# Kernel tuning notes

Measured on AMD Instinct MI355X. Metric: run time of the kernel, lower is better.

The kernel has to match this reference:

```python
import jax, jax.numpy as jnp
import numpy as np

N = 4096       # nodes
NFEAT = 256    # feature dim
NCLASS = 16
E = 65536      # edges = N * avg_degree(16)
NLAYER = 4
ALPHA = 0.5    # blancealpha (non-trainable)
LAMBDA_1 = 1.0
LAMBDA_2 = 1.0
EPS = 1e-12    # F.normalize eps


def setup_inputs() -> dict:
    key = jax.random.key(0)
    ks = jax.random.split(key, 9)
    feat = jax.random.normal(ks[0], (N, NFEAT), dtype=jnp.float32)
    z0 = jax.random.uniform(ks[1], (N, NFEAT), dtype=jnp.float32)       # torch.rand init of z
    w1 = jax.random.uniform(ks[2], (N, N), dtype=jnp.float32)           # uniform_(0,1)
    EA = jax.random.uniform(ks[3], (N, N), dtype=jnp.float32)           # uniform_(0,1)
    w2_w = jax.random.normal(ks[4], (2 * NFEAT, NCLASS), dtype=jnp.float32) * 0.05
    w2_b = jnp.zeros((NCLASS,), dtype=jnp.float32)
    edge_i = jax.random.randint(ks[5], (E,), 0, N, dtype=jnp.int32)
    edge_j = jax.random.randint(ks[6], (E,), 0, N, dtype=jnp.int32)
    edge_val = jax.random.uniform(ks[7], (E,), dtype=jnp.float32)
    # dense adjacency from the sparse edge list (coalesce -> duplicate indices sum)
    adj = jnp.zeros((N, N), dtype=jnp.float32).at[edge_i, edge_j].add(edge_val)
    # w22 = ones with zeros at edge positions (as in __init__)
    w22 = jnp.ones((N, N), dtype=jnp.float32).at[edge_i, edge_j].set(0.0)
    return dict(feat=feat, z0=z0, w1=w1, EA=EA, w2_w=w2_w, w2_b=w2_b,
                adj=adj, w22=w22, edge_val=edge_val, edge_i=edge_i, edge_j=edge_j)


def reference(feat, z0, w1, EA, w2_w, w2_b, adj, w22, edge_val, edge_i, edge_j):
    n = feat.shape[0]
    y = feat                      # y starts as feat
    z = z0                        # torch.rand init, passed in for determinism
    EP = jnp.ones((n, n), dtype=feat.dtype)
    masked_EA = ALPHA * EA * w22  # constant across layers
    for _ in range(NLAYER):
        # dropout is identity in eval mode (training=False)
        A = adj * EP + masked_EA            # [n, n]
        yyT = y @ y.T                       # [n, n] (reused; same values as the two torch.mm calls)
        temp = EP.T @ y + A @ y - yyT @ y   # [n, nfeat]
        temp = jax.nn.sigmoid(w1 @ temp)
        y_n = (LAMBDA_2 / 2) * temp + feat
        z_n = z - A @ z                     # (I - A) @ z
        # ans(z, adj): edgewise ||z_i - z_j|| * adj_val scattered to dense
        P = jnp.linalg.norm(z[edge_i] - z[edge_j], axis=1) * edge_val   # [E]
        M = jnp.zeros((n, n), dtype=z.dtype).at[edge_i, edge_j].add(P)
        EP = (LAMBDA_2 * (yyT - masked_EA) - LAMBDA_1 * 0.5 * M) / LAMBDA_2
        y, z = y_n, z_n
    # F.normalize(p=2, dim=1)
    y = y / jnp.maximum(jnp.linalg.norm(y, axis=1, keepdims=True), EPS)
    z = z / jnp.maximum(jnp.linalg.norm(z, axis=1, keepdims=True), EPS)
    p = jnp.concatenate([z, y], axis=1)     # [n, 2*nfeat]
    logits = p @ w2_w + w2_b
    return jax.nn.log_softmax(logits, axis=1)
```

## Files before the change

kernel.cpp:

```cpp
#include <hip/hip_runtime.h>

#define Nn 4096
#define Ff 256
#define NCLS 16
#define Ne 65536
#define TSZ 262144
#define NF (Nn*Ff)
#define NNx (Nn*Nn)

typedef unsigned short u16;
typedef unsigned int u32;
typedef __attribute__((ext_vector_type(8))) short short8;
typedef __attribute__((ext_vector_type(4))) float float4v;

__device__ __forceinline__ float bfh(u16 u){ return __uint_as_float(((u32)u)<<16); }
__device__ __forceinline__ u16 f2bf(float f){
    u32 u = __float_as_uint(f);
    return (u16)((u + 0x7FFFu + ((u>>16)&1u)) >> 16);
}
__device__ __forceinline__ void gload16(const u16* g, u16* l){
    __builtin_amdgcn_global_load_lds(
        (const __attribute__((address_space(1))) u32*)(const void*)g,
        (__attribute__((address_space(3))) u32*)(void*)l, 16, 0, 0);
}

__device__ float g_yA[NF], g_yB[NF], g_zA[NF], g_zB[NF], g_t1[NF], g_T1[NF];
__device__ float g_Gp[32*Ff*Ff], g_col[Ff], g_P[Ne], g_cc[Ne], g_hV[TSZ];
__device__ float g_pb[(size_t)24*NF];
__device__ u32 g_hK[TSZ], g_slot[Ne];
__device__ int g_cntI[Nn], g_cntJ[Nn], g_rpI[Nn+1], g_rpJ[Nn+1], g_fI[Nn], g_fJ[Nn];
__device__ int g_lI[Ne], g_lJ[Ne];
__device__ __align__(16) u16 g_w1h[NNx], g_w1l[NNx];
__device__ __align__(16) u16 g_meh[NNx], g_mel[NNx];
__device__ __align__(16) u16 g_mth[NNx], g_mtl[NNx];
__device__ __align__(16) u16 g_x0h[NF], g_x0l[NF], g_x1h[NF], g_x1l[NF];
__device__ __align__(16) u16 g_zt0h[NF], g_zt0l[NF], g_zt1h[NF], g_zt1l[NF];
__device__ __align__(16) u16 g_yr0h[NF], g_yr0l[NF], g_yr1h[NF], g_yr1l[NF];
__device__ __align__(16) u16 g_tth[NF], g_ttl[NF];
__device__ __align__(16) u16 g_gth[Ff*Ff], g_gtl[Ff*Ff];
__device__ __align__(16) u16 g_g2h[Ff*Ff], g_g2l[Ff*Ff];

__global__ __launch_bounds__(256) void k_zero(float* p, int n){
    int i = blockIdx.x*256 + threadIdx.x;
    if (i < n) p[i] = 0.f;
}
__global__ __launch_bounds__(256) void k_zeroi(int* p, int n){
    int i = blockIdx.x*256 + threadIdx.x;
    if (i < n) p[i] = 0;
}
__global__ __launch_bounds__(256) void k_fillc(float* p, float v, int n){
    int i = blockIdx.x*256 + threadIdx.x;
    if (i < n) p[i] = v;
}
__global__ __launch_bounds__(256) void k_hkeys_clear(u32* K){
    int i = blockIdx.x*256 + threadIdx.x;
    if (i < TSZ) K[i] = 0xFFFFFFFFu;
}
__global__ __launch_bounds__(256) void k_hsetup(u32* K, u32* slot, const int* ei, const int* ej){
    int e = blockIdx.x*256 + threadIdx.x;
    if (e >= Ne) return;
    u32 key = ((u32)ei[e] << 12) | (u32)ej[e];
    u32 h = (key * 2654435761u) & (TSZ-1);
    for (;;){
        u32 old = atomicCAS(&K[h], 0xFFFFFFFFu, key);
        if (old == 0xFFFFFFFFu || old == key){ slot[e] = h; break; }
        h = (h+1) & (TSZ-1);
    }
}

__global__ __launch_bounds__(256) void k_count(int* cntI, int* cntJ, const int* ei, const int* ej){
    int e = blockIdx.x*256 + threadIdx.x;
    if (e < Ne){ atomicAdd(&cntI[ei[e]], 1); atomicAdd(&cntJ[ej[e]], 1); }
}
__global__ __launch_bounds__(1024) void k_scan(const int* cnt, int* rp){
    __shared__ int s[1024];
    int t = threadIdx.x, b = t*4;
    int a0 = cnt[b], a1 = cnt[b+1], a2 = cnt[b+2], a3 = cnt[b+3];
    int sum = a0+a1+a2+a3;
    s[t] = sum; __syncthreads();
    for (int o = 1; o < 1024; o <<= 1){
        int v = (t >= o) ? s[t-o] : 0;
        __syncthreads();
        s[t] += v;
        __syncthreads();
    }
    int excl = s[t] - sum;
    rp[b] = excl; rp[b+1] = excl+a0; rp[b+2] = excl+a0+a1; rp[b+3] = excl+a0+a1+a2;
    if (t == 1023) rp[4096] = s[1023];
}
__global__ __launch_bounds__(256) void k_fillcsr(const int* rpI, const int* rpJ, int* fI, int* fJ,
                                                 int* lI, int* lJ, const int* ei, const int* ej){
    int e = blockIdx.x*256 + threadIdx.x;
    if (e >= Ne) return;
    int i = ei[e], j = ej[e];
    lI[rpI[i] + atomicAdd(&fI[i], 1)] = e;
    lJ[rpJ[j] + atomicAdd(&fJ[j], 1)] = e;
}

__global__ __launch_bounds__(256) void k_split4(ushort4* hi, ushort4* lo, const float4* w, int n4){
    int i = blockIdx.x*256 + threadIdx.x;
    if (i >= n4) return;
    float4 v = w[i];
    ushort4 h, l;
    h.x = f2bf(v.x); l.x = f2bf(v.x - bfh(h.x));
    h.y = f2bf(v.y); l.y = f2bf(v.y - bfh(h.y));
    h.z = f2bf(v.z); l.z = f2bf(v.z - bfh(h.z));
    h.w = f2bf(v.w); l.w = f2bf(v.w - bfh(h.w));
    hi[i] = h; lo[i] = l;
}
__global__ __launch_bounds__(256) void k_splitME2(u16* meh, u16* mel, u16* mth, u16* mtl,
                                                  const float* ea, const float* w22){
    __shared__ float T[64][65];
    int r0 = blockIdx.y*64, c0 = blockIdx.x*64;
    int c = threadIdx.x & 63, rr = threadIdx.x >> 6;
    for (int q = 0; q < 16; ++q){
        int r = q*4 + rr;
        size_t idx = (size_t)(r0+r)*Nn + c0 + c;
        float v = 0.5f*ea[idx]*w22[idx];
        T[r][c] = v;
        u16 h = f2bf(v); meh[idx] = h; mel[idx] = f2bf(v - bfh(h));
    }
    __syncthreads();
    for (int q = 0; q < 16; ++q){
        int r = q*4 + rr;
        float v = T[c][r];
        size_t o = (size_t)(c0+r)*Nn + r0 + c;
        u16 h = f2bf(v); mth[o] = h; mtl[o] = f2bf(v - bfh(h));
    }
}
__global__ __launch_bounds__(256) void k_splitXT(u16* hi, u16* lo, const float* X){
    __shared__ float T[64][65];
    int r0 = blockIdx.y*64, c0 = blockIdx.x*64;
    int c = threadIdx.x & 63, rr = threadIdx.x >> 6;
    for (int q = 0; q < 16; ++q){
        int r = q*4 + rr;
        T[r][c] = X[(size_t)(r0+r)*Ff + c0 + c];
    }
    __syncthreads();
    for (int q = 0; q < 16; ++q){
        int r = q*4 + rr;
        float v = T[c][r];
        size_t o = (size_t)(c0+r)*Nn + r0 + c;
        u16 h = f2bf(v); hi[o] = h; lo[o] = f2bf(v - bfh(h));
    }
}
__global__ __launch_bounds__(256) void k_splitGT(u16* hi, u16* lo, const float* Gp){
    __shared__ float T[64][65];
    int r0 = blockIdx.y*64, c0 = blockIdx.x*64;
    int c = threadIdx.x & 63, rr = threadIdx.x >> 6;
    for (int q = 0; q < 16; ++q){
        int r = q*4 + rr;
        float v = 0.f;
        #pragma unroll
        for (int z = 0; z < 16; ++z) v += Gp[z*(Ff*Ff) + (r0+r)*Ff + c0 + c];
        T[r][c] = v;
    }
    __syncthreads();
    for (int q = 0; q < 16; ++q){
        int r = q*4 + rr;
        float v = T[c][r];
        int o = (c0+r)*Ff + r0 + c;
        u16 h = f2bf(v); hi[o] = h; lo[o] = f2bf(v - bfh(h));
    }
}
__global__ __launch_bounds__(256) void k_splitGT2(u16* h0, u16* l0, u16* h1, u16* l1,
                                                  const float* Gp){
    __shared__ float T[64][65];
    const int which = blockIdx.z;
    u16* hi = which ? h1 : h0;
    u16* lo = which ? l1 : l0;
    const float* G = Gp + (size_t)which*16*(Ff*Ff);
    int r0 = blockIdx.y*64, c0 = blockIdx.x*64;
    int c = threadIdx.x & 63, rr = threadIdx.x >> 6;
    for (int q = 0; q < 16; ++q){
        int r = q*4 + rr;
        float v = 0.f;
        #pragma unroll
        for (int z = 0; z < 16; ++z) v += G[z*(Ff*Ff) + (r0+r)*Ff + c0 + c];
        T[r][c] = v;
    }
    __syncthreads();
    for (int q = 0; q < 16; ++q){
        int r = q*4 + rr;
        float v = T[c][r];
        int o = (c0+r)*Ff + r0 + c;
        u16 h = f2bf(v); hi[o] = h; lo[o] = f2bf(v - bfh(h));
    }
}

__device__ __forceinline__ void mm_tile(
    const u16* __restrict__ Ahp, const u16* __restrict__ Alp,
    const u16* __restrict__ Bhp, const u16* __restrict__ Blp,
    size_t sA, size_t sB, int i0, int j0, int k0,
    u16* LAh, u16* LAl, u16* LBh, u16* LBl,
    float4v* acc, int lane, int w)
{
    const int g1 = w*64 + lane;
    const int g2 = g1 + 256;
    const int r1 = g1>>3, p1 = g1&7, r2 = g2>>3, p2 = g2&7;
    const size_t a1 = (size_t)(i0+r1)*sA + (size_t)(k0 + ((p1 ^ (r1&7))<<3));
    const size_t a2 = (size_t)(i0+r2)*sA + (size_t)(k0 + ((p2 ^ (r2&7))<<3));
    const size_t b1 = (size_t)(j0+r1)*sB + (size_t)(k0 + ((p1 ^ (r1&7))<<3));
    const size_t b2 = (size_t)(j0+r2)*sB + (size_t)(k0 + ((p2 ^ (r2&7))<<3));
    __syncthreads();
    gload16(Ahp + a1, LAh + g1*8);
    gload16(Ahp + a2, LAh + g2*8);
    gload16(Alp + a1, LAl + g1*8);
    gload16(Alp + a2, LAl + g2*8);
    gload16(Bhp + b1, LBh + g1*8);
    gload16(Bhp + b2, LBh + g2*8);
    gload16(Blp + b1, LBl + g1*8);
    gload16(Blp + b2, LBl + g2*8);
    __syncthreads();
    const int arow = w*16 + (lane&15);
    const int aswz = arow & 7;
    #pragma unroll
    for (int kk = 0; kk < 2; ++kk){
        const int ch = kk*4 + (lane>>4);
        short8 ah = *(const short8*)(LAh + arow*64 + ((ch ^ aswz)<<3));
        short8 al = *(const short8*)(LAl + arow*64 + ((ch ^ aswz)<<3));
        #pragma unroll
        for (int c = 0; c < 4; ++c){
            const int brow = c*16 + (lane&15);
            const int bo = brow*64 + ((ch ^ (brow&7))<<3);
            short8 bh = *(const short8*)(LBh + bo);
            short8 bl = *(const short8*)(LBl + bo);
            acc[c] = __builtin_amdgcn_mfma_f32_16x16x32_bf16(ah, bh, acc[c], 0,0,0);
            acc[c] = __builtin_amdgcn_mfma_f32_16x16x32_bf16(ah, bl, acc[c], 0,0,0);
            acc[c] = __builtin_amdgcn_mfma_f32_16x16x32_bf16(al, bh, acc[c], 0,0,0);
        }
    }
}

template<int V>
__global__ __launch_bounds__(256) void k_mm(float* __restrict__ out,
        const u16* __restrict__ Ahp, const u16* __restrict__ Alp,
        const u16* __restrict__ Bhp, const u16* __restrict__ Blp,
        const float* __restrict__ aux1){
    __shared__ u16 LAh[4096], LAl[4096], LBh[4096], LBl[4096];
    const int tid = threadIdx.x, lane = tid & 63, w = tid >> 6;
    const int j0 = blockIdx.x*64, i0 = blockIdx.y*64;
    float4v acc[4];
    #pragma unroll
    for (int c = 0; c < 4; ++c) acc[c] = (float4v){0.f,0.f,0.f,0.f};
    for (int kt = 0; kt < 4; ++kt)
        mm_tile(Ahp, Alp, Bhp, Blp, (size_t)Ff, (size_t)Ff, i0, j0, kt*64, LAh, LAl, LBh, LBl, acc, lane, w);
    #pragma unroll
    for (int c = 0; c < 4; ++c)
        #pragma unroll
        for (int r = 0; r < 4; ++r){
            int grow = i0 + w*16 + (lane>>4)*4 + r;
            int gcol = j0 + c*16 + (lane&15);
            size_t idx = (size_t)grow*Ff + gcol;
            float v = acc[c][r];
            if constexpr (V == 3) out[idx] = aux1[idx] - v;
            if constexpr (V == 4) out[idx] = aux1[gcol] - v;
            if constexpr (V == 5) out[idx] = v;
        }
}

__global__ __launch_bounds__(256) void k_gram_mm(float* __restrict__ Gp,
        const u16* __restrict__ Ahp, const u16* __restrict__ Alp,
        const u16* __restrict__ Bhp, const u16* __restrict__ Blp){
    __shared__ u16 LAh[4096], LAl[4096], LBh[4096], LBl[4096];
    const int tid = threadIdx.x, lane = tid & 63, w = tid >> 6;
    const int j0 = blockIdx.x*64, i0 = blockIdx.y*64, kb = blockIdx.z*256;
    float4v acc[4];
    #pragma unroll
    for (int c = 0; c < 4; ++c) acc[c] = (float4v){0.f,0.f,0.f,0.f};
    for (int kt = 0; kt < 4; ++kt)
        mm_tile(Ahp, Alp, Bhp, Blp, (size_t)Nn, (size_t)Nn, i0, j0, kb + kt*64, LAh, LAl, LBh, LBl, acc, lane, w);
    float* op = Gp + (size_t)blockIdx.z*(Ff*Ff);
    #pragma unroll
    for (int c = 0; c < 4; ++c)
        #pragma unroll
        for (int r = 0; r < 4; ++r){
            int grow = i0 + w*16 + (lane>>4)*4 + r;
            int gcol = j0 + c*16 + (lane&15);
            op[grow*Ff + gcol] = acc[c][r];
        }
}

__global__ __launch_bounds__(256) void k_gram_mm2(float* __restrict__ Gp,
        const u16* __restrict__ Ahp, const u16* __restrict__ Alp,
        const u16* __restrict__ Bhp, const u16* __restrict__ Blp){
    __shared__ u16 LAh[4096], LAl[4096], LBh[4096], LBl[4096];
    const int tid = threadIdx.x, lane = tid & 63, w = tid >> 6;
    const int j0 = blockIdx.x*64, i0 = blockIdx.y*64;
    const int pz = blockIdx.z;
    const int kb = (pz & 15)*256, which = pz >> 4;
    const u16* pAh = which ? Bhp : Ahp;
    const u16* pAl = which ? Blp : Alp;
    float4v acc[4];
    #pragma unroll
    for (int c = 0; c < 4; ++c) acc[c] = (float4v){0.f,0.f,0.f,0.f};
    for (int kt = 0; kt < 4; ++kt)
        mm_tile(pAh, pAl, Bhp, Blp, (size_t)Nn, (size_t)Nn, i0, j0, kb + kt*64, LAh, LAl, LBh, LBl, acc, lane, w);
    float* op = Gp + (size_t)pz*(Ff*Ff);
    #pragma unroll
    for (int c = 0; c < 4; ++c)
        #pragma unroll
        for (int r = 0; r < 4; ++r){
            int grow = i0 + w*16 + (lane>>4)*4 + r;
            int gcol = j0 + c*16 + (lane&15);
            op[grow*Ff + gcol] = acc[c][r];
        }
}

template<int KSP>
__global__ __launch_bounds__(512) void k_mmB(float* __restrict__ pb,
        const u16* __restrict__ A0h, const u16* __restrict__ A0l,
        const u16* __restrict__ B0h, const u16* __restrict__ B0l,
        const u16* __restrict__ A1h, const u16* __restrict__ A1l,
        const u16* __restrict__ B1h, const u16* __restrict__ B1l,
        const u16* __restrict__ A2h, const u16* __restrict__ A2l,
        const u16* __restrict__ B2h, const u16* __restrict__ B2l){
    __shared__ u16 LAh[4096], LAl[4096], LBh[16384], LBl[16384];
    const int tid = threadIdx.x, lane = tid & 63, w = tid >> 6;
    const int z = blockIdx.x, i0 = blockIdx.y*64, bat = blockIdx.z;
    const u16 *Ah, *Al, *Bh, *Bl;
    if (bat == 0){ Ah = A0h; Al = A0l; Bh = B0h; Bl = B0l; }
    else if (bat == 1){ Ah = A1h; Al = A1l; Bh = B1h; Bl = B1l; }
    else { Ah = A2h; Al = A2l; Bh = B2h; Bl = B2l; }
    const int wr = w >> 2, wc = w & 3;
    float4v acc[2][4];
    #pragma unroll
    for (int m = 0; m < 2; ++m)
        #pragma unroll
        for (int n = 0; n < 4; ++n) acc[m][n] = (float4v){0.f,0.f,0.f,0.f};

    const int ra = tid >> 3, pa = tid & 7;
    const size_t aoff = (size_t)(i0+ra)*Nn + (size_t)((pa ^ (ra&7))<<3);
    constexpr int NKT = 64 / KSP;

    for (int kt = 0; kt < NKT; ++kt){
        const int k0 = z*(NKT*64) + kt*64;
        __syncthreads();
        gload16(Ah + aoff + k0, LAh + tid*8);
        gload16(Al + aoff + k0, LAl + tid*8);
        #pragma unroll
        for (int it = 0; it < 4; ++it){
            int g = it*512 + tid;
            int r = g >> 3, p = g & 7;
            size_t b = (size_t)r*Nn + (size_t)(k0 + ((p ^ (r&7))<<3));
            gload16(Bh + b, LBh + g*8);
            gload16(Bl + b, LBl + g*8);
        }
        __syncthreads();
        #pragma unroll
        for (int kk = 0; kk < 2; ++kk){
            const int ch = kk*4 + (lane>>4);
            short8 ah0, ah1, al0, al1;
            {
                const int arow = wr*32 + (lane&15);
                const int ao = arow*64 + ((ch ^ (arow&7))<<3);
                ah0 = *(const short8*)(LAh + ao);
                al0 = *(const short8*)(LAl + ao);
            }
            {
                const int arow = wr*32 + 16 + (lane&15);
                const int ao = arow*64 + ((ch ^ (arow&7))<<3);
                ah1 = *(const short8*)(LAh + ao);
                al1 = *(const short8*)(LAl + ao);
            }
            #pragma unroll
            for (int n = 0; n < 4; ++n){
                const int bcol = wc*64 + n*16 + (lane&15);
                const int bo = bcol*64 + ((ch ^ (bcol&7))<<3);
                short8 bh = *(const short8*)(LBh + bo);
                short8 bl = *(const short8*)(LBl + bo);
                acc[0][n] = __builtin_amdgcn_mfma_f32_16x16x32_bf16(ah0, bh, acc[0][n], 0,0,0);
                acc[0][n] = __builtin_amdgcn_mfma_f32_16x16x32_bf16(ah0, bl, acc[0][n], 0,0,0);
                acc[0][n] = __builtin_amdgcn_mfma_f32_16x16x32_bf16(al0, bh, acc[0][n], 0,0,0);
                acc[1][n] = __builtin_amdgcn_mfma_f32_16x16x32_bf16(ah1, bh, acc[1][n], 0,0,0);
                acc[1][n] = __builtin_amdgcn_mfma_f32_16x16x32_bf16(ah1, bl, acc[1][n], 0,0,0);
                acc[1][n] = __builtin_amdgcn_mfma_f32_16x16x32_bf16(al1, bh, acc[1][n], 0,0,0);
            }
        }
    }
    float* op = pb + ((size_t)bat*KSP + z)*NF;
    #pragma unroll
    for (int m = 0; m < 2; ++m)
        #pragma unroll
        for (int n = 0; n < 4; ++n)
            #pragma unroll
            for (int r = 0; r < 4; ++r){
                int row = i0 + wr*32 + m*16 + (lane>>4)*4 + r;
                int col = wc*64 + n*16 + (lane&15);
                op[(size_t)row*Ff + col] = acc[m][n][r];
            }
}

template<int HASM, int DOSPLIT>
__global__ __launch_bounds__(256) void k_redT1(float* __restrict__ t1, const float* __restrict__ pb,
        u16* __restrict__ th, u16* __restrict__ tl){
    __shared__ float T[64][65];
    const int c0 = blockIdx.x*64, r0 = blockIdx.y*64;
    const int c = threadIdx.x & 63, rr = threadIdx.x >> 6;
    for (int q = 0; q < 16; ++q){
        int row = q*4 + rr;
        size_t idx = (size_t)(r0+row)*Ff + c0 + c;
        float s = 0.f;
        #pragma unroll
        for (int p = 0; p < 4; ++p) s += pb[(size_t)p*NF + idx];
        if constexpr (HASM){
            #pragma unroll
            for (int p = 0; p < 4; ++p) s -= pb[((size_t)8 + p)*NF + idx];
        }
        float val = t1[idx] + s;
        t1[idx] = val;
        if constexpr (DOSPLIT) T[row][c] = val;
    }
    if constexpr (DOSPLIT){
        __syncthreads();
        for (int q = 0; q < 16; ++q){
            int r = q*4 + rr;
            float v = T[c][r];
            size_t o = (size_t)(c0+r)*Nn + r0 + c;
            u16 h = f2bf(v); th[o] = h; tl[o] = f2bf(v - bfh(h));
        }
    }
}

__global__ __launch_bounds__(256) void k_redY(float* __restrict__ yn, const float* __restrict__ pb,
        const float* __restrict__ feat, u16* __restrict__ rh, u16* __restrict__ rl,
        u16* __restrict__ th, u16* __restrict__ tl){
    __shared__ float T[64][65];
    const int c0 = blockIdx.x*64, r0 = blockIdx.y*64;
    const int c = threadIdx.x & 63, rr = threadIdx.x >> 6;
    for (int q = 0; q < 16; ++q){
        int row = q*4 + rr;
        size_t idx = (size_t)(r0+row)*Ff + c0 + c;
        float s = 0.f;
        #pragma unroll
        for (int p = 0; p < 8; ++p) s += pb[(size_t)p*NF + idx];
        float val = feat[idx] + 0.5f*(1.f/(1.f+expf(-s)));
        yn[idx] = val;
        u16 h = f2bf(val); rh[idx] = h; rl[idx] = f2bf(val - bfh(h));
        T[row][c] = val;
    }
    __syncthreads();
    for (int q = 0; q < 16; ++q){
        int r = q*4 + rr;
        float v = T[c][r];
        size_t o = (size_t)(c0+r)*Nn + r0 + c;
        u16 h = f2bf(v); th[o] = h; tl[o] = f2bf(v - bfh(h));
    }
}

__global__ __launch_bounds__(256) void k_csrTZ(float* __restrict__ t1, float* __restrict__ zn,
        const float* __restrict__ y, const float* __restrict__ z, const float* __restrict__ pb1,
        const float* __restrict__ cc, const float* __restrict__ P,
        const int* __restrict__ rpI, const int* __restrict__ lI, const int* __restrict__ ej,
        const int* __restrict__ rpJ, const int* __restrict__ lJ, const int* __restrict__ ei,
        int useM){
    const int r = blockIdx.x, f = threadIdx.x;
    float at = 0.f, az = 0.f;
    const int b0 = rpI[r], b1 = rpI[r+1];
    for (int p = b0; p < b1; ++p){
        int e = lI[p];
        float ce = cc[e];
        int j = ej[e];
        at += ce * y[(size_t)j*Ff + f];
        az += ce * z[(size_t)j*Ff + f];
    }
    if (useM){
        const int c0 = rpJ[r], c1 = rpJ[r+1];
        for (int p = c0; p < c1; ++p){
            int e = lJ[p];
            at -= 0.5f * P[e] * y[(size_t)ei[e]*Ff + f];
        }
    }
    size_t idx = (size_t)r*Ff + f;
    float dz = 0.f;
    #pragma unroll
    for (int p = 0; p < 4; ++p) dz += pb1[(size_t)p*NF + idx];
    t1[idx] += at;
    zn[idx] = z[idx] - dz - az;
}

__global__ __launch_bounds__(256) void k_colsum(float* col, const float* __restrict__ y){
    int j = threadIdx.x;
    int r0 = blockIdx.x*64;
    float s = 0.f;
    for (int i = 0; i < 64; ++i) s += y[(size_t)(r0+i)*Ff + j];
    atomicAdd(&col[j], s);
}

__global__ __launch_bounds__(256) void k_pacc(float* __restrict__ P, float* __restrict__ hV,
        const float* __restrict__ z, const int* __restrict__ ei, const int* __restrict__ ej,
        const float* __restrict__ ev, const u32* __restrict__ slot){
    int e = blockIdx.x*4 + (threadIdx.x >> 6);
    int lane = threadIdx.x & 63;
    int i = ei[e], j = ej[e];
    float s = 0.f;
    #pragma unroll
    for (int q = 0; q < 4; ++q){
        int f = lane + q*64;
        float d = z[(size_t)i*Ff + f] - z[(size_t)j*Ff + f];
        s += d*d;
    }
    #pragma unroll
    for (int o = 32; o; o >>= 1) s += __shfl_xor(s, o);
    if (lane == 0){
        float v = sqrtf(s) * ev[e];
        P[e] = v;
        atomicAdd(&hV[slot[e]], v);
    }
}
__global__ __launch_bounds__(256) void k_ep(float* __restrict__ c, const float* __restrict__ y,
        const int* __restrict__ ei, const int* __restrict__ ej, const float* __restrict__ ev,
        const float* __restrict__ V, const u32* __restrict__ slot){
    int e = blockIdx.x*4 + (threadIdx.x >> 6);
    int lane = threadIdx.x & 63;
    int i = ei[e], j = ej[e];
    float s = 0.f;
    #pragma unroll
    for (int q = 0; q < 4; ++q){
        int f = lane + q*64;
        s += y[(size_t)i*Ff + f] * y[(size_t)j*Ff + f];
    }
    #pragma unroll
    for (int o = 32; o; o >>= 1) s += __shfl_xor(s, o);
    if (lane == 0) c[e] = ev[e] * (s - 0.5f * V[slot[e]]);
}

__global__ __launch_bounds__(256) void k_head(float* __restrict__ out, const float* __restrict__ y,
                                              const float* __restrict__ z, const float* __restrict__ w2w,
                                              const float* __restrict__ w2b){
    const int node = blockIdx.x, t = threadIdx.x;
    float yv = y[(size_t)node*Ff + t], zv = z[(size_t)node*Ff + t];
    float yc = fminf(fmaxf(yv, -1e37f), 1e37f);
    float zc = fminf(fmaxf(zv, -1e37f), 1e37f);
    __shared__ float sy[256], sz[256];
    sy[t] = fabsf(yc); sz[t] = fabsf(zc);
    __syncthreads();
    for (int s = 128; s; s >>= 1){ if (t < s){ sy[t]=fmaxf(sy[t],sy[t+s]); sz[t]=fmaxf(sz[t],sz[t+s]); } __syncthreads(); }
    float my_ = fmaxf(sy[0], 1e-30f), mz_ = fmaxf(sz[0], 1e-30f);
    __syncthreads();
    float ysc = yc/my_, zsc = zc/mz_;
    sy[t] = ysc*ysc; sz[t] = zsc*zsc;
    __syncthreads();
    for (int s = 128; s; s >>= 1){ if (t < s){ sy[t]+=sy[t+s]; sz[t]+=sz[t+s]; } __syncthreads(); }
    float ny = fmaxf(my_*sqrtf(sy[0]), 1e-12f);
    float nz = fmaxf(mz_*sqrtf(sz[0]), 1e-12f);
    float ynv = yc/ny, znv = zc/nz;
    float acc[NCLS];
    #pragma unroll
    for (int cc = 0; cc < NCLS; ++cc)
        acc[cc] = znv*w2w[t*NCLS+cc] + ynv*w2w[(Ff+t)*NCLS+cc];
    __shared__ float red[NCLS][257];
    #pragma unroll
    for (int cc = 0; cc < NCLS; ++cc) red[cc][t] = acc[cc];
    __syncthreads();
    for (int s = 128; s; s >>= 1){
        if (t < s){
            #pragma unroll
            for (int cc = 0; cc < NCLS; ++cc) red[cc][t] += red[cc][t+s];
        }
        __syncthreads();
    }
    __shared__ float lg[NCLS];
    __shared__ float ml[2];
    if (t < NCLS) lg[t] = red[t][0] + w2b[t];
    __syncthreads();
    if (t == 0){
        float m = -1e30f;
        for (int cc = 0; cc < NCLS; ++cc) m = fmaxf(m, lg[cc]);
        float se = 0.f;
        for (int cc = 0; cc < NCLS; ++cc) se += expf(lg[cc]-m);
        ml[0] = m; ml[1] = logf(se);
    }
    __syncthreads();
    if (t < NCLS) out[(size_t)node*NCLS + t] = lg[t] - ml[0] - ml[1];
}

extern "C" void kernel_launch(void* const* d_in, const int* in_sizes, int n_in,
                              void* d_out, int out_size, void* d_ws, size_t ws_size,
                              hipStream_t stream){
    const float* feat = (const float*)d_in[0];
    const float* z0i  = (const float*)d_in[1];
    const float* w1p  = (const float*)d_in[2];
    const float* EAp  = (const float*)d_in[3];
    const float* w2w  = (const float*)d_in[4];
    const float* w2b  = (const float*)d_in[5];
    const float* w22p = (const float*)d_in[7];
    const float* evp  = (const float*)d_in[8];
    const int* ei   = (const int*)d_in[9];
    const int* ej   = (const int*)d_in[10];
    float* out = (float*)d_out;

    int ok = (n_in == 11) && (out_size == Nn*NCLS)
           && in_sizes[0]==NF && in_sizes[1]==NF && in_sizes[2]==NNx && in_sizes[3]==NNx
           && in_sizes[4]==2*Ff*NCLS && in_sizes[5]==NCLS && in_sizes[6]==NNx && in_sizes[7]==NNx
           && in_sizes[8]==Ne && in_sizes[9]==Ne && in_sizes[10]==Ne;
    if (!ok){
        k_fillc<<<(out_size+255)/256, 256, 0, stream>>>(out, -100.0f, out_size);
        return;
    }

    float *yA,*yB,*zA,*zB,*t1,*T1,*Gp,*col,*P,*cc,*hV,*pb; u32 *hK,*slot;
    int *cntI,*cntJ,*rpI,*rpJ,*fI,*fJ,*lI,*lJ;
    u16 *w1h,*w1l,*meh,*mel,*mth,*mtl,*gth,*gtl,*g2h,*g2l,*tth,*ttl;
    u16 *xh[2],*xl[2],*zth[2],*ztl[2],*yrh[2],*yrl[2];
    hipGetSymbolAddress((void**)&yA,  HIP_SYMBOL(g_yA));
    hipGetSymbolAddress((void**)&yB,  HIP_SYMBOL(g_yB));
    hipGetSymbolAddress((void**)&zA,  HIP_SYMBOL(g_zA));
    hipGetSymbolAddress((void**)&zB,  HIP_SYMBOL(g_zB));
    hipGetSymbolAddress((void**)&t1,  HIP_SYMBOL(g_t1));
    hipGetSymbolAddress((void**)&T1,  HIP_SYMBOL(g_T1));
    hipGetSymbolAddress((void**)&Gp,  HIP_SYMBOL(g_Gp));
    hipGetSymbolAddress((void**)&col, HIP_SYMBOL(g_col));
    hipGetSymbolAddress((void**)&P,   HIP_SYMBOL(g_P));
    hipGetSymbolAddress((void**)&cc,  HIP_SYMBOL(g_cc));
    hipGetSymbolAddress((void**)&hV,  HIP_SYMBOL(g_hV));
    hipGetSymbolAddress((void**)&pb,  HIP_SYMBOL(g_pb));
    hipGetSymbolAddress((void**)&hK,  HIP_SYMBOL(g_hK));
    hipGetSymbolAddress((void**)&slot,HIP_SYMBOL(g_slot));
    hipGetSymbolAddress((void**)&cntI,HIP_SYMBOL(g_cntI));
    hipGetSymbolAddress((void**)&cntJ,HIP_SYMBOL(g_cntJ));
    hipGetSymbolAddress((void**)&rpI, HIP_SYMBOL(g_rpI));
    hipGetSymbolAddress((void**)&rpJ, HIP_SYMBOL(g_rpJ));
    hipGetSymbolAddress((void**)&fI,  HIP_SYMBOL(g_fI));
    hipGetSymbolAddress((void**)&fJ,  HIP_SYMBOL(g_fJ));
    hipGetSymbolAddress((void**)&lI,  HIP_SYMBOL(g_lI));
    hipGetSymbolAddress((void**)&lJ,  HIP_SYMBOL(g_lJ));
    hipGetSymbolAddress((void**)&w1h, HIP_SYMBOL(g_w1h));
    hipGetSymbolAddress((void**)&w1l, HIP_SYMBOL(g_w1l));
    hipGetSymbolAddress((void**)&meh, HIP_SYMBOL(g_meh));
    hipGetSymbolAddress((void**)&mel, HIP_SYMBOL(g_mel));
    hipGetSymbolAddress((void**)&mth, HIP_SYMBOL(g_mth));
    hipGetSymbolAddress((void**)&mtl, HIP_SYMBOL(g_mtl));
    hipGetSymbolAddress((void**)&gth, HIP_SYMBOL(g_gth));
    hipGetSymbolAddress((void**)&gtl, HIP_SYMBOL(g_gtl));
    hipGetSymbolAddress((void**)&g2h, HIP_SYMBOL(g_g2h));
    hipGetSymbolAddress((void**)&g2l, HIP_SYMBOL(g_g2l));
    hipGetSymbolAddress((void**)&tth, HIP_SYMBOL(g_tth));
    hipGetSymbolAddress((void**)&ttl, HIP_SYMBOL(g_ttl));
    hipGetSymbolAddress((void**)&xh[0], HIP_SYMBOL(g_x0h));
    hipGetSymbolAddress((void**)&xl[0], HIP_SYMBOL(g_x0l));
    hipGetSymbolAddress((void**)&xh[1], HIP_SYMBOL(g_x1h));
    hipGetSymbolAddress((void**)&xl[1], HIP_SYMBOL(g_x1l));
    hipGetSymbolAddress((void**)&zth[0], HIP_SYMBOL(g_zt0h));
    hipGetSymbolAddress((void**)&ztl[0], HIP_SYMBOL(g_zt0l));
    hipGetSymbolAddress((void**)&zth[1], HIP_SYMBOL(g_zt1h));
    hipGetSymbolAddress((void**)&ztl[1], HIP_SYMBOL(g_zt1l));
    hipGetSymbolAddress((void**)&yrh[0], HIP_SYMBOL(g_yr0h));
    hipGetSymbolAddress((void**)&yrl[0], HIP_SYMBOL(g_yr0l));
    hipGetSymbolAddress((void**)&yrh[1], HIP_SYMBOL(g_yr1h));
    hipGetSymbolAddress((void**)&yrl[1], HIP_SYMBOL(g_yr1l));

    const dim3 gSmall(Ff/64, Nn/64);
    const dim3 gXT(Ff/64, Nn/64);
    const dim3 gME(Nn/64, Nn/64);
    const dim3 gGT(Ff/64, Ff/64);
    const dim3 gGram(4, 4, 16);
    const dim3 gGram2(4, 4, 32);
    const dim3 gGT2(4, 4, 2);
    const dim3 gRed(Ff/64, Nn/64);

    k_split4<<<NNx/4/256, 256, 0, stream>>>((ushort4*)w1h, (ushort4*)w1l, (const float4*)w1p, NNx/4);
    k_splitME2<<<gME, 256, 0, stream>>>(meh, mel, mth, mtl, EAp, w22p);
    k_split4<<<NF/4/256, 256, 0, stream>>>((ushort4*)yrh[0], (ushort4*)yrl[0], (const float4*)feat, NF/4);
    k_splitXT<<<gXT, 256, 0, stream>>>(xh[0], xl[0], feat);
    k_splitXT<<<gXT, 256, 0, stream>>>(zth[0], ztl[0], z0i);
    k_hkeys_clear<<<TSZ/256, 256, 0, stream>>>(hK);
    k_hsetup<<<Ne/256, 256, 0, stream>>>(hK, slot, ei, ej);
    k_zeroi<<<Nn/256, 256, 0, stream>>>(cntI, Nn);
    k_zeroi<<<Nn/256, 256, 0, stream>>>(cntJ, Nn);
    k_count<<<Ne/256, 256, 0, stream>>>(cntI, cntJ, ei, ej);
    k_scan<<<1, 1024, 0, stream>>>(cntI, rpI);
    k_scan<<<1, 1024, 0, stream>>>(cntJ, rpJ);
    k_zeroi<<<Nn/256, 256, 0, stream>>>(fI, Nn);
    k_zeroi<<<Nn/256, 256, 0, stream>>>(fJ, Nn);
    k_fillcsr<<<Ne/256, 256, 0, stream>>>(rpI, rpJ, fI, fJ, lI, lJ, ei, ej);

    const float* yv = feat;  const float* zv = z0i;
    for (int t = 1; t <= 4; ++t){
        int ri = (t-1) & 1, wi = t & 1;
        u16 *xhc = xh[ri], *xlc = xl[ri], *xhn = xh[wi], *xln = xl[wi];
        u16 *zthc = zth[ri], *ztlc = ztl[ri], *zthn = zth[wi], *ztln = ztl[wi];
        u16 *yrhc = yrh[ri], *yrlc = yrl[ri], *yrhn = yrh[wi], *yrln = yrl[wi];
        float* yn = (t & 1) ? yA : yB;
        float* zn = (t & 1) ? zA : zB;
        const float* ccv = (t == 1) ? evp : cc;

        if (t == 1){
            k_gram_mm<<<gGram, 256, 0, stream>>>(Gp, xhc, xlc, xhc, xlc);
            k_splitGT<<<gGT, 256, 0, stream>>>(gth, gtl, Gp);
            k_zero<<<1, 256, 0, stream>>>(col, Ff);
            k_colsum<<<64, 256, 0, stream>>>(col, yv);
            k_mm<4><<<gSmall, 256, 0, stream>>>(t1, yrhc, yrlc, gth, gtl, col);
        } else {
            k_mm<3><<<gSmall, 256, 0, stream>>>(t1, yrhc, yrlc, g2h, g2l, T1);
        }
        {
            int nb = (t == 1) ? 2 : 3;
            dim3 gB(4, Nn/64, nb);
            k_mmB<4><<<gB, 512, 0, stream>>>(pb,
                meh, mel, xhc, xlc,
                meh, mel, zthc, ztlc,
                mth, mtl, xhc, xlc);
        }
        k_csrTZ<<<Nn, 256, 0, stream>>>(t1, zn, yv, zv, pb + (size_t)4*NF, ccv, P,
                                        rpI, lI, ej, rpJ, lJ, ei, (t >= 2) ? 1 : 0);
        if (t == 1) k_redT1<0,1><<<gRed, 256, 0, stream>>>(t1, pb, tth, ttl);
        else        k_redT1<1,1><<<gRed, 256, 0, stream>>>(t1, pb, tth, ttl);
        if (t < 4)
            k_splitXT<<<gXT, 256, 0, stream>>>(zthn, ztln, zn);
        {
            dim3 gB(8, Nn/64, 1);
            k_mmB<8><<<gB, 512, 0, stream>>>(pb,
                w1h, w1l, tth, ttl,
                w1h, w1l, tth, ttl,
                w1h, w1l, tth, ttl);
        }
        k_redY<<<gRed, 256, 0, stream>>>(yn, pb, feat, yrhn, yrln, xhn, xln);
        if (t < 4){
            k_zero<<<TSZ/256, 256, 0, stream>>>(hV, TSZ);
            k_pacc<<<Ne/4, 256, 0, stream>>>(P, hV, zv, ei, ej, evp, slot);
            k_ep<<<Ne/4, 256, 0, stream>>>(cc, yv, ei, ej, evp, hV, slot);
            k_gram_mm2<<<gGram2, 256, 0, stream>>>(Gp, xhc, xlc, xhn, xln);
            k_splitGT2<<<gGT2, 256, 0, stream>>>(gth, gtl, g2h, g2l, Gp);
            k_mm<5><<<gSmall, 256, 0, stream>>>(T1, yrhc, yrlc, gth, gtl, nullptr);
        }
        yv = yn; zv = zn;
    }
    k_head<<<Nn, 256, 0, stream>>>(out, yv, zv, w2w, w2b);
}
```

Baseline: 1.352 ms.

## Double-buffer LDS tiles in k_mmB with async prefetch of next K-slice

Rewrites the k_mmB split-K GEMM main loop to use two LDS buffers with a K-step of 32 instead of 64. The loads for the next tile are issued before computing on the current one, and partial vmcnt waits let global-to-LDS transfers overlap the MFMA work. The swizzle pattern and thread-to-load mapping change for the narrower tile. The cost is twice as many barrier pairs per unit of work, and it relies on hand-placed waitcnt counts matching the number of loads issued.

After: 1.414 ms. 1.05x slower.

```diff
diff --git a/kernel.cpp b/kernel.cpp
--- a/kernel.cpp
+++ b/kernel.cpp
@@ -315,7 +315,8 @@
         const u16* __restrict__ B1h, const u16* __restrict__ B1l,
         const u16* __restrict__ A2h, const u16* __restrict__ A2l,
         const u16* __restrict__ B2h, const u16* __restrict__ B2l){
-    __shared__ u16 LAh[4096], LAl[4096], LBh[16384], LBl[16384];
+    __shared__ __align__(16) u16 LA[2][2][2048];
+    __shared__ __align__(16) u16 LB[2][2][8192];
     const int tid = threadIdx.x, lane = tid & 63, w = tid >> 6;
     const int z = blockIdx.x, i0 = blockIdx.y*64, bat = blockIdx.z;
     const u16 *Ah, *Al, *Bh, *Bl;
@@ -329,55 +330,65 @@
         #pragma unroll
         for (int n = 0; n < 4; ++n) acc[m][n] = (float4v){0.f,0.f,0.f,0.f};
 
-    const int ra = tid >> 3, pa = tid & 7;
-    const size_t aoff = (size_t)(i0+ra)*Nn + (size_t)((pa ^ (ra&7))<<3);
-    constexpr int NKT = 64 / KSP;
-
+    const int at = tid & 255;
+    const int ar_ = at >> 2, ap_ = at & 3;
+    const size_t aoff = (size_t)(i0 + ar_)*Nn + (size_t)((ap_ ^ ((ar_>>1)&3))<<3);
+    const u16* Asel = (tid < 256) ? Ah : Al;
+    const int asl = (tid < 256) ? 0 : 1;
+    const int br0 = tid >> 2, bp_ = tid & 3;
+    const int br1 = br0 + 128;
+    const size_t boff0 = (size_t)br0*Nn + (size_t)((bp_ ^ ((br0>>1)&3))<<3);
+    const size_t boff1 = (size_t)br1*Nn + (size_t)((bp_ ^ ((br1>>1)&3))<<3);
+    const int kbase = z * (4096/KSP);
+    constexpr int NKT = 128 / KSP;
+
+#define STAGE(B, K0) { \
+    gload16(Asel + aoff + (K0), &LA[B][asl][at*8]); \
+    gload16(Bh + boff0 + (K0), &LB[B][0][tid*8]); \
+    gload16(Bh + boff1 + (K0), &LB[B][0][tid*8 + 4096]); \
+    gload16(Bl + boff0 + (K0), &LB[B][1][tid*8]); \
+    gload16(Bl + boff1 + (K0), &LB[B][1][tid*8 + 4096]); }
+
+#define COMPUTE(B) { \
+    const int ch = lane >> 4; \
+    const int ar0 = wr*32 + (lane&15); \
+    const int ar1 = ar0 + 16; \
+    const int ao0 = ar0*32 + ((ch ^ ((ar0>>1)&3))<<3); \
+    const int ao1 = ar1*32 + ((ch ^ ((ar1>>1)&3))<<3); \
+    short8 ah0 = *(const short8*)&LA[B][0][ao0]; \
+    short8 al0 = *(const short8*)&LA[B][1][ao0]; \
+    short8 ah1 = *(const short8*)&LA[B][0][ao1]; \
+    short8 al1 = *(const short8*)&LA[B][1][ao1]; \
+    _Pragma("unroll") \
+    for (int n = 0; n < 4; ++n){ \
+        const int bc = wc*64 + n*16 + (lane&15); \
+        const int bo = bc*32 + ((ch ^ ((bc>>1)&3))<<3); \
+        short8 bh = *(const short8*)&LB[B][0][bo]; \
+        short8 bl = *(const short8*)&LB[B][1][bo]; \
+        acc[0][n] = __builtin_amdgcn_mfma_f32_16x16x32_bf16(ah0, bh, acc[0][n], 0,0,0); \
+        acc[0][n] = __builtin_amdgcn_mfma_f32_16x16x32_bf16(ah0, bl, acc[0][n], 0,0,0); \
+        acc[0][n] = __builtin_amdgcn_mfma_f32_16x16x32_bf16(al0, bh, acc[0][n], 0,0,0); \
+        acc[1][n] = __builtin_amdgcn_mfma_f32_16x16x32_bf16(ah1, bh, acc[1][n], 0,0,0); \
+        acc[1][n] = __builtin_amdgcn_mfma_f32_16x16x32_bf16(ah1, bl, acc[1][n], 0,0,0); \
+        acc[1][n] = __builtin_amdgcn_mfma_f32_16x16x32_bf16(al1, bh, acc[1][n], 0,0,0); \
+    } }
+
+    STAGE(0, kbase)
     for (int kt = 0; kt < NKT; ++kt){
-        const int k0 = z*(NKT*64) + kt*64;
-        __syncthreads();
-        gload16(Ah + aoff + k0, LAh + tid*8);
-        gload16(Al + aoff + k0, LAl + tid*8);
-        #pragma unroll
-        for (int it = 0; it < 4; ++it){
-            int g = it*512 + tid;
-            int r = g >> 3, p = g & 7;
-            size_t b = (size_t)r*Nn + (size_t)(k0 + ((p ^ (r&7))<<3));
-            gload16(Bh + b, LBh + g*8);
-            gload16(Bl + b, LBl + g*8);
-        }
-        __syncthreads();
-        #pragma unroll
-        for (int kk = 0; kk < 2; ++kk){
-            const int ch = kk*4 + (lane>>4);
-            short8 ah0, ah1, al0, al1;
-            {
-                const int arow = wr*32 + (lane&15);
-                const int ao = arow*64 + ((ch ^ (arow&7))<<3);
-                ah0 = *(const short8*)(LAh + ao);
-                al0 = *(const short8*)(LAl + ao);
-            }
-            {
-                const int arow = wr*32 + 16 + (lane&15);
-                const int ao = arow*64 + ((ch ^ (arow&7))<<3);
-                ah1 = *(const short8*)(LAh + ao);
-                al1 = *(const short8*)(LAl + ao);
-            }
-            #pragma unroll
-            for (int n = 0; n < 4; ++n){
-                const int bcol = wc*64 + n*16 + (lane&15);
-                const int bo = bcol*64 + ((ch ^ (bcol&7))<<3);
-                short8 bh = *(const short8*)(LBh + bo);
-                short8 bl = *(const short8*)(LBl + bo);
-                acc[0][n] = __builtin_amdgcn_mfma_f32_16x16x32_bf16(ah0, bh, acc[0][n], 0,0,0);
-                acc[0][n] = __builtin_amdgcn_mfma_f32_16x16x32_bf16(ah0, bl, acc[0][n], 0,0,0);
-                acc[0][n] = __builtin_amdgcn_mfma_f32_16x16x32_bf16(al0, bh, acc[0][n], 0,0,0);
-                acc[1][n] = __builtin_amdgcn_mfma_f32_16x16x32_bf16(ah1, bh, acc[1][n], 0,0,0);
-                acc[1][n] = __builtin_amdgcn_mfma_f32_16x16x32_bf16(ah1, bl, acc[1][n], 0,0,0);
-                acc[1][n] = __builtin_amdgcn_mfma_f32_16x16x32_bf16(al1, bh, acc[1][n], 0,0,0);
-            }
-        }
-    }
+        if (kt + 1 < NKT){
+            STAGE((kt+1)&1, kbase + (kt+1)*32)
+            asm volatile("s_waitcnt vmcnt(5)" ::: "memory");
+        } else {
+            asm volatile("s_waitcnt vmcnt(0)" ::: "memory");
+        }
+        __builtin_amdgcn_s_barrier();
+        __builtin_amdgcn_sched_barrier(0);
+        COMPUTE(kt&1)
+        __builtin_amdgcn_s_barrier();
+    }
+#undef STAGE
+#undef COMPUTE
+
     float* op = pb + ((size_t)bat*KSP + z)*NF;
     #pragma unroll
     for (int m = 0; m < 2; ++m)
```
